# Kernel optimization log

Hardware: AMD Instinct MI355X
Metric: run time of the kernel (lower is better)

Reference implementation:

```python
import jax, jax.numpy as jnp
import numpy as np

B, N, DIM, H, DH = 8, 1024, 512, 8, 64
INNER = H * DH
SCALE = DH ** -0.5


def setup_inputs() -> dict:
    key = jax.random.key(0)
    ks = jax.random.split(key, 9)
    s = 0.02
    return {
        "x": jax.random.normal(ks[0], (B, N, DIM), jnp.float32),
        "lidar": jax.random.normal(ks[1], (B, N, INNER), jnp.float32),
        "w_qkv": jax.random.normal(ks[2], (3 * INNER, DIM), jnp.float32) * s,
        "w_merge": jax.random.normal(ks[3], (DH, DH), jnp.float32) * s,
        "b_merge": jnp.zeros((DH,), jnp.float32),
        "w_out": jax.random.normal(ks[4], (DIM, INNER), jnp.float32) * s,
        "b_out": jnp.zeros((DIM,), jnp.float32),
        "conv_w": jax.random.normal(ks[5], (2,), jnp.float32) * 0.5,
        "conv_b": jnp.zeros((), jnp.float32),
    }


def _split_heads(t):  # [b, n, h*d] -> [b, h, n, d]
    b, n, _ = t.shape
    return t.reshape(b, n, H, DH).transpose(0, 2, 1, 3)


def reference(x, lidar, w_qkv, w_merge, b_merge, w_out, b_out, conv_w, conv_b):
    b, n, _ = x.shape
    qkv = x @ w_qkv.T  # [b, n, 3*inner]
    q, k, v = jnp.split(qkv, 3, axis=-1)
    q, k, v = _split_heads(q), _split_heads(k), _split_heads(v)
    lid = _split_heads(lidar)

    dots = jnp.einsum('bhid,bhjd->bhij', q, k) * SCALE
    lidar_sim = jnp.einsum('bhid,bhjd->bhij', lid, lid) * SCALE
    lidar_sim = jax.nn.softmax(lidar_sim, axis=-1)

    # 1x1 conv over 2 channels == learned linear blend of the two score maps
    mid = conv_w[0] * dots + conv_w[1] * lidar_sim + conv_b
    attn = jax.nn.softmax(mid, axis=-1)

    out = jnp.einsum('bhij,bhjd->bhid', attn, v)
    out = out @ w_merge.T + b_merge                  # per-head linear_merge
    out = out.transpose(0, 2, 1, 3).reshape(b, n, INNER)  # b h n d -> b n (h d)
    out = out @ w_out.T + b_out                      # to_out (dropout = identity)
    return (out, lidar)
```

## Files before the change

### kernel.cpp

```cpp
#include <hip/hip_runtime.h>
#include <hip/hip_bf16.h>

#define B_      8
#define N_      1024
#define DIM_    512
#define H_      8
#define DH_     64
#define INNER_  512
#define SCALE_  0.125f
#define LOG2E_  1.4426950408889634f

typedef __attribute__((ext_vector_type(8))) __bf16         bf16x8;
typedef __attribute__((ext_vector_type(8))) unsigned short ushort8;
typedef __attribute__((ext_vector_type(4))) float          f32x4;

union FragCast { ushort8 u; bf16x8 b; };
union FragU32  { unsigned int u[4]; bf16x8 b; };

__device__ inline bf16x8 ld_frag(const unsigned short* p) {
    FragCast f; f.u = *(const ushort8*)p; return f.b;
}

__device__ inline f32x4 mfma16(bf16x8 a, bf16x8 b, f32x4 c) {
    return __builtin_amdgcn_mfma_f32_16x16x32_bf16(a, b, c, 0, 0, 0);
}

__device__ inline float fexp2(float x) { return __builtin_amdgcn_exp2f(x); }

__device__ inline unsigned short f2bf(float x) {
    unsigned int u = __float_as_uint(x);
    unsigned int lsb = (u >> 16) & 1u;
    u += 0x7fffu + lsb;
    return (unsigned short)(u >> 16);
}

__device__ inline unsigned int pack_bf2(float hi, float lo) {
    return __builtin_amdgcn_perm(__float_as_uint(hi), __float_as_uint(lo), 0x07060302u);
}

__device__ inline void gl_lds(const unsigned short* g, unsigned short* l) {
    __builtin_amdgcn_global_load_lds(
        (const __attribute__((address_space(1))) unsigned int*)g,
        (__attribute__((address_space(3))) unsigned int*)l, 16, 0, 0);
}

__global__ __launch_bounds__(256) void k_convert(
    const float* __restrict__ x, const float* __restrict__ lidar,
    const float* __restrict__ wqkv, const float* __restrict__ wmerge,
    const float* __restrict__ wout,
    unsigned short* __restrict__ x_bf, unsigned short* __restrict__ lid_bf,
    float* __restrict__ out_lidar,
    unsigned short* __restrict__ wqkv_bf, unsigned short* __restrict__ wm_bf,
    unsigned short* __restrict__ wout_bf)
{
    const int bx = blockIdx.x, tid = threadIdx.x;
    const float* src; unsigned short* dst; bool isLid = false; long base;
    if (bx < 1024)      { src = x;      dst = x_bf;    base = (long)bx * 1024; }
    else if (bx < 2048) { src = lidar;  dst = lid_bf;  base = (long)(bx - 1024) * 1024; isLid = true; }
    else if (bx < 2240) { src = wqkv;   dst = wqkv_bf; base = (long)(bx - 2048) * 1024; }
    else if (bx < 2304) { src = wout;   dst = wout_bf; base = (long)(bx - 2240) * 1024; }
    else                { src = wmerge; dst = wm_bf;   base = 0; }
    for (int k = 0; k < 4; k++) {
        long j = base + k * 256 + tid;
        float4 v = ((const float4*)src)[j];
        ushort4 o;
        o.x = f2bf(v.x); o.y = f2bf(v.y); o.z = f2bf(v.z); o.w = f2bf(v.w);
        ((ushort4*)dst)[j] = o;
        if (isLid) ((float4*)out_lidar)[j] = v;
    }
}

__global__ __launch_bounds__(256) void k_gemm_qkv(
    const unsigned short* __restrict__ A, const unsigned short* __restrict__ Bm,
    unsigned short* __restrict__ C, unsigned short* __restrict__ vt,
    int M, int Nd, int K)
{
    __shared__ unsigned short sA[128 * 64];
    __shared__ unsigned short sB[128 * 64];
    const int tid  = threadIdx.x;
    const int lane = tid & 63, wave = tid >> 6;
    const int q = lane >> 4, l15 = lane & 15, l7 = l15 & 7;
    const int xq0 = (q ^ l7) << 3, xq4 = ((q + 4) ^ l7) << 3;
    const int m0 = blockIdx.x * 128, n0 = blockIdx.y * 128;
    const int wm = (wave >> 1) * 64, wn = (wave & 1) * 64;
    f32x4 acc[4][4] = {};

    for (int k0 = 0; k0 < K; k0 += 64) {
        __syncthreads();
        for (int i = 0; i < 4; i++) {
            int c = i * 256 + tid;
            int row = c >> 3;
            int gcol = ((c & 7) ^ (row & 7)) << 3;
            gl_lds(&A[(long)(m0 + row) * K + k0 + gcol], &sA[c * 8]);
            gl_lds(&Bm[(long)(n0 + row) * K + k0 + gcol], &sB[c * 8]);
        }
        __syncthreads();
        for (int kk = 0; kk < 2; kk++) {
            const int xx = kk ? xq4 : xq0;
            bf16x8 af[4], bfr[4];
            for (int i = 0; i < 4; i++)
                af[i]  = ld_frag(&sA[(wm + i * 16 + l15) * 64 + xx]);
            for (int i = 0; i < 4; i++)
                bfr[i] = ld_frag(&sB[(wn + i * 16 + l15) * 64 + xx]);
            for (int mi = 0; mi < 4; mi++)
                for (int ni = 0; ni < 4; ni++)
                    acc[mi][ni] = mfma16(af[mi], bfr[ni], acc[mi][ni]);
        }
    }
    if (n0 < 1024) {
        for (int mi = 0; mi < 4; mi++)
            for (int ni = 0; ni < 4; ni++)
                for (int r = 0; r < 4; r++) {
                    int row = m0 + wm + mi * 16 + q * 4 + r;
                    int col = n0 + wn + ni * 16 + l15;
                    C[(long)row * Nd + col] = f2bf(acc[mi][ni][r]);
                }
    } else {
        for (int mi = 0; mi < 4; mi++) {
            int pp0 = (mi >> 1) * 32 + q * 8 + (mi & 1) * 4;
            long tbase = m0 + wm + pp0;
            for (int ni = 0; ni < 4; ni++) {
                int f = (n0 - 1024) + wn + ni * 16 + l15;
                ushort4 o4;
                o4.x = f2bf(acc[mi][ni][0]); o4.y = f2bf(acc[mi][ni][1]);
                o4.z = f2bf(acc[mi][ni][2]); o4.w = f2bf(acc[mi][ni][3]);
                *(ushort4*)&vt[(long)f * (B_ * N_) + tbase] = o4;
            }
        }
    }
}

__global__ __launch_bounds__(256) void k_gemm_out(
    const unsigned short* __restrict__ A, const unsigned short* __restrict__ Bm,
    const float* __restrict__ bias, float* __restrict__ C, int M, int Nd, int K)
{
    __shared__ unsigned short sA[128 * 64];
    __shared__ unsigned short sB[64 * 64];
    const int tid  = threadIdx.x;
    const int lane = tid & 63, wave = tid >> 6;
    const int q = lane >> 4, l15 = lane & 15, l7 = l15 & 7;
    const int xq0 = (q ^ l7) << 3, xq4 = ((q + 4) ^ l7) << 3;
    const int m0 = blockIdx.x * 128, n0 = blockIdx.y * 64;
    const int wm = (wave >> 1) * 64, wn = (wave & 1) * 32;
    f32x4 acc[4][2] = {};

    for (int k0 = 0; k0 < K; k0 += 64) {
        __syncthreads();
        for (int i = 0; i < 4; i++) {
            int c = i * 256 + tid;
            int row = c >> 3;
            int gcol = ((c & 7) ^ (row & 7)) << 3;
            gl_lds(&A[(long)(m0 + row) * K + k0 + gcol], &sA[c * 8]);
            if (i < 2)
                gl_lds(&Bm[(long)(n0 + row) * K + k0 + gcol], &sB[c * 8]);
        }
        __syncthreads();
        for (int kk = 0; kk < 2; kk++) {
            const int xx = kk ? xq4 : xq0;
            bf16x8 af[4], bfr[2];
            for (int i = 0; i < 4; i++)
                af[i]  = ld_frag(&sA[(wm + i * 16 + l15) * 64 + xx]);
            for (int i = 0; i < 2; i++)
                bfr[i] = ld_frag(&sB[(wn + i * 16 + l15) * 64 + xx]);
            for (int mi = 0; mi < 4; mi++)
                for (int ni = 0; ni < 2; ni++)
                    acc[mi][ni] = mfma16(af[mi], bfr[ni], acc[mi][ni]);
        }
    }
    for (int mi = 0; mi < 4; mi++)
        for (int ni = 0; ni < 2; ni++)
            for (int r = 0; r < 4; r++) {
                int row = m0 + wm + mi * 16 + q * 4 + r;
                int col = n0 + wn + ni * 16 + l15;
                C[(long)row * Nd + col] = acc[mi][ni][r] + bias[col];
            }
}

__global__ __launch_bounds__(256) void k_flash(
    const unsigned short* __restrict__ qkv_bf, const unsigned short* __restrict__ lid_bf,
    const unsigned short* __restrict__ vt,
    const unsigned short* __restrict__ wm_bf, const float* __restrict__ b_merge,
    const float* __restrict__ conv_w, const float* __restrict__ conv_b,
    unsigned short* __restrict__ tmp_bf)
{
    __shared__ unsigned short sK[64 * 64];
    __shared__ unsigned short sLid[64 * 64];
    __shared__ unsigned short sVT[64 * 64];
    __shared__ unsigned short sO[4 * 16 * 72];
    __shared__ float sRS[4][16];

    const int tid = threadIdx.x, lane = tid & 63, wave = tid >> 6;
    const int q = lane >> 4, l15 = lane & 15, l7 = l15 & 7;
    const int xq0 = (q ^ l7) << 3, xq4 = ((q + 4) ^ l7) << 3;
    const int bh = blockIdx.x, itile = blockIdx.y;
    const int b = bh >> 3, h = bh & 7;
    const int i0w = itile * 64 + wave * 16;
    const long rowB = (long)b * N_;
    const int colh = h * DH_;
    const float k0c = conv_w[0] * SCALE_ * LOG2E_;
    const float k2c = conv_b[0] * LOG2E_;
    const float c1L = conv_w[1] * LOG2E_;
    const float sc = SCALE_ * LOG2E_;

    bf16x8 qf[2], lfq[2];
    for (int ks = 0; ks < 2; ks++) {
        qf[ks]  = ld_frag(&qkv_bf[(rowB + i0w + l15) * 1536 + colh + ks * 32 + q * 8]);
        lfq[ks] = ld_frag(&lid_bf[(rowB + i0w + l15) * INNER_ + colh + ks * 32 + q * 8]);
    }

    float rsl = 0.f;
    for (int j0 = 0; j0 < N_; j0 += 64) {
        __syncthreads();
        for (int i = 0; i < 2; i++) {
            int c = i * 256 + tid;
            int row = c >> 3;
            int gcol = ((c & 7) ^ (row & 7)) << 3;
            gl_lds(&lid_bf[(rowB + j0 + row) * INNER_ + colh + gcol], &sLid[c * 8]);
        }
        __syncthreads();
        for (int ns = 0; ns < 4; ns++) {
            int rb = (ns * 16 + l15) * 64;
            f32x4 cv = {0.f, 0.f, 0.f, 0.f};
            cv = mfma16(ld_frag(&sLid[rb + xq0]), lfq[0], cv);
            cv = mfma16(ld_frag(&sLid[rb + xq4]), lfq[1], cv);
            for (int r = 0; r < 4; r++) rsl += fexp2(cv[r] * sc);
        }
    }
    rsl += __shfl_xor(rsl, 16);
    rsl += __shfl_xor(rsl, 32);
    const float k1 = c1L / rsl;

    float rs = 0.f;
    f32x4 o[4] = {};

    for (int j0 = 0; j0 < N_; j0 += 64) {
        __syncthreads();
        for (int i = 0; i < 2; i++) {
            int c = i * 256 + tid;
            int row = c >> 3;
            int gcol = ((c & 7) ^ (row & 7)) << 3;
            gl_lds(&qkv_bf[(rowB + j0 + row) * 1536 + 512 + colh + gcol], &sK[c * 8]);
            gl_lds(&lid_bf[(rowB + j0 + row) * INNER_ + colh + gcol], &sLid[c * 8]);
            gl_lds(&vt[(long)(colh + row) * (B_ * N_) + rowB + j0 + gcol], &sVT[c * 8]);
        }
        __syncthreads();

        for (int ns2 = 0; ns2 < 2; ns2++) {
            FragU32 fa;
            for (int h2 = 0; h2 < 2; h2++) {
                int ns = ns2 * 2 + h2;
                int rb = (ns * 16 + l15) * 64;
                f32x4 a = {0.f, 0.f, 0.f, 0.f};
                a = mfma16(ld_frag(&sK[rb + xq0]), qf[0], a);
                a = mfma16(ld_frag(&sK[rb + xq4]), qf[1], a);
                f32x4 cv = {0.f, 0.f, 0.f, 0.f};
                cv = mfma16(ld_frag(&sLid[rb + xq0]), lfq[0], cv);
                cv = mfma16(ld_frag(&sLid[rb + xq4]), lfq[1], cv);
                float pv[4];
                for (int r = 0; r < 4; r++) {
                    float els = fexp2(cv[r] * sc);
                    float t = fmaf(k0c, a[r], k2c);
                    t = fmaf(k1, els, t);
                    pv[r] = fexp2(t);
                    rs += pv[r];
                }
                fa.u[h2 * 2 + 0] = pack_bf2(pv[1], pv[0]);
                fa.u[h2 * 2 + 1] = pack_bf2(pv[3], pv[2]);
            }
            for (int dt = 0; dt < 4; dt++) {
                int vrow = dt * 16 + l15;
                bf16x8 vb = ld_frag(&sVT[vrow * 64 + (((ns2 * 4 + q) ^ l7) << 3)]);
                o[dt] = mfma16(fa.b, vb, o[dt]);
            }
        }
    }

    rs += __shfl_xor(rs, 16);
    rs += __shfl_xor(rs, 32);
    if (q == 0) sRS[wave][l15] = rs;
    float invr[4];
    for (int r = 0; r < 4; r++) invr[r] = 1.f / sRS[wave][q * 4 + r];

    unsigned short* pO = &sO[wave * 16 * 72];
    for (int dt = 0; dt < 4; dt++)
        for (int r = 0; r < 4; r++)
            pO[(q * 4 + r) * 72 + dt * 16 + l15] = f2bf(o[dt][r] * invr[r]);

    f32x4 mo[4] = {};
    for (int ks = 0; ks < 2; ks++) {
        bf16x8 af = ld_frag(&pO[l15 * 72 + ks * 32 + q * 8]);
        for (int ns = 0; ns < 4; ns++) {
            bf16x8 wf = ld_frag(&wm_bf[(ns * 16 + l15) * 64 + ks * 32 + q * 8]);
            mo[ns] = mfma16(af, wf, mo[ns]);
        }
    }
    for (int ns = 0; ns < 4; ns++) {
        float bm = b_merge[ns * 16 + l15];
        for (int r = 0; r < 4; r++) {
            long row = rowB + i0w + q * 4 + r;
            tmp_bf[row * INNER_ + colh + ns * 16 + l15] = f2bf(mo[ns][r] + bm);
        }
    }
}

extern "C" void kernel_launch(void* const* d_in, const int* in_sizes, int n_in,
                              void* d_out, int out_size, void* d_ws, size_t ws_size,
                              hipStream_t stream) {
    const float* x       = (const float*)d_in[0];
    const float* lidar   = (const float*)d_in[1];
    const float* w_qkv   = (const float*)d_in[2];
    const float* w_merge = (const float*)d_in[3];
    const float* b_merge = (const float*)d_in[4];
    const float* w_out   = (const float*)d_in[5];
    const float* b_out   = (const float*)d_in[6];
    const float* conv_w  = (const float*)d_in[7];
    const float* conv_b  = (const float*)d_in[8];

    float* out0      = (float*)d_out;
    float* out_lidar = out0 + (long)B_ * N_ * INNER_;

    size_t off = 0;
    auto carve = [&](size_t bytes) {
        void* p = (char*)d_ws + off;
        off += (bytes + 255) & ~(size_t)255;
        return p;
    };
    unsigned short* qkv_bf  = (unsigned short*)carve((size_t)B_ * N_ * 3 * INNER_ * 2);
    unsigned short* lid_bf  = (unsigned short*)carve((size_t)B_ * N_ * INNER_ * 2);
    unsigned short* x_bf    = (unsigned short*)carve((size_t)B_ * N_ * DIM_ * 2);
    unsigned short* wqkv_bf = (unsigned short*)carve((size_t)3 * INNER_ * DIM_ * 2);
    unsigned short* wout_bf = (unsigned short*)carve((size_t)DIM_ * INNER_ * 2);
    unsigned short* wm_bf   = (unsigned short*)carve((size_t)DH_ * DH_ * 2);
    unsigned short* tmp_bf  = (unsigned short*)carve((size_t)B_ * N_ * INNER_ * 2);
    unsigned short* vt_bf   = (unsigned short*)carve((size_t)INNER_ * B_ * N_ * 2);

    k_convert<<<2305, 256, 0, stream>>>(x, lidar, w_qkv, w_merge, w_out,
                                        x_bf, lid_bf, out_lidar,
                                        wqkv_bf, wm_bf, wout_bf);

    k_gemm_qkv<<<dim3(64, 12), 256, 0, stream>>>(
        x_bf, wqkv_bf, qkv_bf, vt_bf, B_ * N_, 3 * INNER_, DIM_);

    k_flash<<<dim3(64, 16), 256, 0, stream>>>(
        qkv_bf, lid_bf, vt_bf, wm_bf, b_merge, conv_w, conv_b, tmp_bf);

    k_gemm_out<<<dim3(64, 8), 256, 0, stream>>>(
        tmp_bf, wout_bf, b_out, out0, B_ * N_, DIM_, INNER_);
}
```

Before: 198.6 us.

## Stage V-transpose epilogue through LDS and hoist attention load address math

The QKV GEMM's V-transpose epilogue now writes accumulators into a padded shared buffer, then issues coalesced 16-byte stores to the transposed V array instead of scattered 8-byte stores. The attention kernel precomputes global and LDS pointers for its tile loads and advances them by a fixed stride each iteration, removing per-iteration index arithmetic. The GEMM block's shared memory grows slightly and gains two extra barriers in the V branch.

```diff
diff --git a/kernel.cpp b/kernel.cpp
--- a/kernel.cpp
+++ b/kernel.cpp
@@ -75,8 +75,9 @@
     unsigned short* __restrict__ C, unsigned short* __restrict__ vt,
     int M, int Nd, int K)
 {
-    __shared__ unsigned short sA[128 * 64];
-    __shared__ unsigned short sB[128 * 64];
+    __shared__ unsigned short sMem[128 * 136];
+    unsigned short* sA = sMem;
+    unsigned short* sB = sMem + 128 * 64;
     const int tid  = threadIdx.x;
     const int lane = tid & 63, wave = tid >> 6;
     const int q = lane >> 4, l15 = lane & 15, l7 = l15 & 7;
@@ -116,16 +117,27 @@
                     C[(long)row * Nd + col] = f2bf(acc[mi][ni][r]);
                 }
     } else {
+        __syncthreads();
         for (int mi = 0; mi < 4; mi++) {
-            int pp0 = (mi >> 1) * 32 + q * 8 + (mi & 1) * 4;
-            long tbase = m0 + wm + pp0;
+            int t0 = wm + mi * 16 + q * 4;
             for (int ni = 0; ni < 4; ni++) {
-                int f = (n0 - 1024) + wn + ni * 16 + l15;
+                int f = wn + ni * 16 + l15;
                 ushort4 o4;
                 o4.x = f2bf(acc[mi][ni][0]); o4.y = f2bf(acc[mi][ni][1]);
                 o4.z = f2bf(acc[mi][ni][2]); o4.w = f2bf(acc[mi][ni][3]);
-                *(ushort4*)&vt[(long)f * (B_ * N_) + tbase] = o4;
-            }
+                *(ushort4*)&sMem[f * 136 + t0] = o4;
+            }
+        }
+        __syncthreads();
+        const long fb = (long)(n0 - 1024) * (B_ * N_) + m0;
+        for (int i = 0; i < 8; i++) {
+            int g = i * 256 + tid;
+            int f = g >> 4, grp = g & 15;
+            int base = (grp >> 2) * 32 + (grp & 3) * 4;
+            ushort4 a4 = *(const ushort4*)&sMem[f * 136 + base];
+            ushort4 b4 = *(const ushort4*)&sMem[f * 136 + base + 16];
+            ushort8 o8 = {a4.x, a4.y, a4.z, a4.w, b4.x, b4.y, b4.z, b4.w};
+            *(ushort8*)&vt[fb + (long)f * (B_ * N_) + grp * 8] = o8;
         }
     }
 }
@@ -202,6 +214,26 @@
     const float c1L = conv_w[1] * LOG2E_;
     const float sc = SCALE_ * LOG2E_;
 
+    int c0i = tid, c1i = 256 + tid;
+    int row0 = c0i >> 3, row1 = c1i >> 3;
+    int gc0 = ((c0i & 7) ^ (row0 & 7)) << 3;
+    int gc1 = ((c1i & 7) ^ (row1 & 7)) << 3;
+    unsigned short* dK0 = &sK[c0i * 8];   unsigned short* dK1 = &sK[c1i * 8];
+    unsigned short* dL0 = &sLid[c0i * 8]; unsigned short* dL1 = &sLid[c1i * 8];
+    unsigned short* dV0 = &sVT[c0i * 8];  unsigned short* dV1 = &sVT[c1i * 8];
+    const unsigned short* gK0 = &qkv_bf[(rowB + row0) * 1536 + 512 + colh + gc0];
+    const unsigned short* gK1 = &qkv_bf[(rowB + row1) * 1536 + 512 + colh + gc1];
+    const unsigned short* gL0 = &lid_bf[(rowB + row0) * INNER_ + colh + gc0];
+    const unsigned short* gL1 = &lid_bf[(rowB + row1) * INNER_ + colh + gc1];
+    const unsigned short* gV0 = &vt[(long)(colh + row0) * (B_ * N_) + rowB + gc0];
+    const unsigned short* gV1 = &vt[(long)(colh + row1) * (B_ * N_) + rowB + gc1];
+
+    const unsigned short *sK_r[4], *sL_r[4];
+    for (int ns = 0; ns < 4; ns++) {
+        sK_r[ns] = &sK[(ns * 16 + l15) * 64];
+        sL_r[ns] = &sLid[(ns * 16 + l15) * 64];
+    }
+
     bf16x8 qf[2], lfq[2];
     for (int ks = 0; ks < 2; ks++) {
         qf[ks]  = ld_frag(&qkv_bf[(rowB + i0w + l15) * 1536 + colh + ks * 32 + q * 8]);
@@ -209,21 +241,21 @@
     }
 
     float rsl = 0.f;
-    for (int j0 = 0; j0 < N_; j0 += 64) {
-        __syncthreads();
-        for (int i = 0; i < 2; i++) {
-            int c = i * 256 + tid;
-            int row = c >> 3;
-            int gcol = ((c & 7) ^ (row & 7)) << 3;
-            gl_lds(&lid_bf[(rowB + j0 + row) * INNER_ + colh + gcol], &sLid[c * 8]);
-        }
-        __syncthreads();
-        for (int ns = 0; ns < 4; ns++) {
-            int rb = (ns * 16 + l15) * 64;
-            f32x4 cv = {0.f, 0.f, 0.f, 0.f};
-            cv = mfma16(ld_frag(&sLid[rb + xq0]), lfq[0], cv);
-            cv = mfma16(ld_frag(&sLid[rb + xq4]), lfq[1], cv);
-            for (int r = 0; r < 4; r++) rsl += fexp2(cv[r] * sc);
+    {
+        const unsigned short* p0 = gL0;
+        const unsigned short* p1 = gL1;
+        for (int j0 = 0; j0 < N_; j0 += 64) {
+            __syncthreads();
+            gl_lds(p0, dL0);
+            gl_lds(p1, dL1);
+            p0 += 64 * INNER_; p1 += 64 * INNER_;
+            __syncthreads();
+            for (int ns = 0; ns < 4; ns++) {
+                f32x4 cv = {0.f, 0.f, 0.f, 0.f};
+                cv = mfma16(ld_frag(sL_r[ns] + xq0), lfq[0], cv);
+                cv = mfma16(ld_frag(sL_r[ns] + xq4), lfq[1], cv);
+                for (int r = 0; r < 4; r++) rsl += fexp2(cv[r] * sc);
+            }
         }
     }
     rsl += __shfl_xor(rsl, 16);
@@ -235,27 +267,24 @@
 
     for (int j0 = 0; j0 < N_; j0 += 64) {
         __syncthreads();
-        for (int i = 0; i < 2; i++) {
-            int c = i * 256 + tid;
-            int row = c >> 3;
-            int gcol = ((c & 7) ^ (row & 7)) << 3;
-            gl_lds(&qkv_bf[(rowB + j0 + row) * 1536 + 512 + colh + gcol], &sK[c * 8]);
-            gl_lds(&lid_bf[(rowB + j0 + row) * INNER_ + colh + gcol], &sLid[c * 8]);
-            gl_lds(&vt[(long)(colh + row) * (B_ * N_) + rowB + j0 + gcol], &sVT[c * 8]);
-        }
+        gl_lds(gK0, dK0); gl_lds(gK1, dK1);
+        gl_lds(gL0, dL0); gl_lds(gL1, dL1);
+        gl_lds(gV0, dV0); gl_lds(gV1, dV1);
+        gK0 += 64 * 1536;  gK1 += 64 * 1536;
+        gL0 += 64 * INNER_; gL1 += 64 * INNER_;
+        gV0 += 64;          gV1 += 64;
         __syncthreads();
 
         for (int ns2 = 0; ns2 < 2; ns2++) {
             FragU32 fa;
             for (int h2 = 0; h2 < 2; h2++) {
                 int ns = ns2 * 2 + h2;
-                int rb = (ns * 16 + l15) * 64;
                 f32x4 a = {0.f, 0.f, 0.f, 0.f};
-                a = mfma16(ld_frag(&sK[rb + xq0]), qf[0], a);
-                a = mfma16(ld_frag(&sK[rb + xq4]), qf[1], a);
+                a = mfma16(ld_frag(sK_r[ns] + xq0), qf[0], a);
+                a = mfma16(ld_frag(sK_r[ns] + xq4), qf[1], a);
                 f32x4 cv = {0.f, 0.f, 0.f, 0.f};
-                cv = mfma16(ld_frag(&sLid[rb + xq0]), lfq[0], cv);
-                cv = mfma16(ld_frag(&sLid[rb + xq4]), lfq[1], cv);
+                cv = mfma16(ld_frag(sL_r[ns] + xq0), lfq[0], cv);
+                cv = mfma16(ld_frag(sL_r[ns] + xq4), lfq[1], cv);
                 float pv[4];
                 for (int r = 0; r < 4; r++) {
                     float els = fexp2(cv[r] * sc);
```

Measured after the change: 193.8 us. 1.02x faster.
